# Optimization experiments

Measured on AMD Instinct MI355X. Metric: run time of the kernel, lower is better.

The kernel has to match this reference:

```python
import jax, jax.numpy as jnp
import numpy as np

B = 512
IMG = 32
NFF = 64
LAT_N = 256
LAT_C = 100
TOKEN_DIM = 3 + 2 * NFF  # 131
HEADS = 4
DEPTH = 2
MLP_HID = 4 * LAT_C
EPS = 1e-5


def _layernorm(x, g, b):
    mu = jnp.mean(x, axis=-1, keepdims=True)
    var = jnp.mean((x - mu) ** 2, axis=-1, keepdims=True)
    return (x - mu) * jax.lax.rsqrt(var + EPS) * g + b


def _mha(h, in_w, in_b, out_w, out_b):
    # torch nn.MultiheadAttention, batch_first, eval mode (no dropout)
    Bh, L, D = h.shape
    hd = D // HEADS
    qkv = h @ in_w.T + in_b  # [B, L, 3D]
    q, k, v = jnp.split(qkv, 3, axis=-1)
    def heads(t):
        return t.reshape(Bh, L, HEADS, hd).transpose(0, 2, 1, 3)  # [B,H,L,hd]
    q, k, v = heads(q), heads(k), heads(v)
    scores = jnp.einsum('bhqd,bhkd->bhqk', q, k) / jnp.sqrt(jnp.float32(hd))
    attn = jax.nn.softmax(scores, axis=-1)
    o = jnp.einsum('bhqk,bhkd->bhqd', attn, v)
    o = o.transpose(0, 2, 1, 3).reshape(Bh, L, D)
    return o @ out_w.T + out_b


def _forward(x, latents, latent_pos, fourier_matrix, proj_w, proj_b,
             q_w, q_b, k_w, k_b, v_w, v_b, o_w, o_b,
             ln1_g, ln1_b, attn_in_w, attn_in_b, attn_out_w, attn_out_b,
             ln2_g, ln2_b, mlp_w1, mlp_b1, mlp_w2, mlp_b2):
    Bx = x.shape[0]
    lat = (latents + latent_pos)[None].repeat(Bx, axis=0)  # [B, 256, 100]

    # per-pixel RGB tokens
    rgb = x.transpose(0, 2, 3, 1).reshape(Bx, -1, 3)  # [B, 1024, 3]

    # Fourier positional encoding
    yy, xx = jnp.meshgrid(jnp.arange(IMG, dtype=jnp.float32),
                          jnp.arange(IMG, dtype=jnp.float32), indexing='ij')
    coords = jnp.stack([xx / (IMG - 1), yy / (IMG - 1)], axis=-1).reshape(-1, 2)  # [1024, 2]
    proj = coords @ fourier_matrix  # [1024, NFF]
    pos = jnp.concatenate([jnp.cos(2 * jnp.pi * proj), jnp.sin(2 * jnp.pi * proj)], axis=-1)
    pos = jnp.broadcast_to(pos[None], (Bx, IMG * IMG, 2 * NFF))

    tokens = jnp.concatenate([rgb, pos], axis=-1)  # [B, 1024, 131]
    tokens = tokens @ proj_w.T + proj_b  # [B, 1024, 100]

    # K/V depend only on (fixed) tokens, identical across the 8 iterations
    k = tokens @ k_w.T + k_b
    v = tokens @ v_w.T + v_b

    scale = 1.0 / jnp.sqrt(jnp.float32(LAT_C))
    for _ in range(8):
        q = lat @ q_w.T + q_b  # [B, 256, 100]
        attn = jax.nn.softmax(jnp.einsum('bqc,bkc->bqk', q, k) * scale, axis=-1)
        lat = jnp.einsum('bqk,bkc->bqc', attn, v) @ o_w.T + o_b
        # latent transformer (depth=2, shared across the 8 iterations)
        for d in range(DEPTH):
            h = _layernorm(lat, ln1_g[d], ln1_b[d])
            lat = lat + _mha(h, attn_in_w[d], attn_in_b[d], attn_out_w[d], attn_out_b[d])
            h = _layernorm(lat, ln2_g[d], ln2_b[d])
            h = jax.nn.gelu(h @ mlp_w1[d].T + mlp_b1[d], approximate=False) @ mlp_w2[d].T + mlp_b2[d]
            lat = lat + h
    return lat.mean(axis=1)  # [B, 100]


def setup_inputs() -> dict:
    key = jax.random.key(0)
    ks = jax.random.split(key, 32)
    s = 0.02
    inp = {
        'x': jax.random.normal(ks[0], (B, 3, IMG, IMG), jnp.float32),
        'latents': jax.random.normal(ks[1], (LAT_N, LAT_C), jnp.float32),
        'latent_pos': jax.random.normal(ks[2], (LAT_N, LAT_C), jnp.float32),
        'fourier_matrix': jax.random.normal(ks[3], (2, NFF), jnp.float32),
        'proj_w': jax.random.normal(ks[4], (LAT_C, TOKEN_DIM), jnp.float32) * s,
        'proj_b': jnp.zeros((LAT_C,), jnp.float32),
        'q_w': jax.random.normal(ks[5], (LAT_C, LAT_C), jnp.float32) * s,
        'q_b': jnp.zeros((LAT_C,), jnp.float32),
        'k_w': jax.random.normal(ks[6], (LAT_C, LAT_C), jnp.float32) * s,
        'k_b': jnp.zeros((LAT_C,), jnp.float32),
        'v_w': jax.random.normal(ks[7], (LAT_C, LAT_C), jnp.float32) * s,
        'v_b': jnp.zeros((LAT_C,), jnp.float32),
        'o_w': jax.random.normal(ks[8], (LAT_C, LAT_C), jnp.float32) * s,
        'o_b': jnp.zeros((LAT_C,), jnp.float32),
        'ln1_g': jnp.ones((DEPTH, LAT_C), jnp.float32),
        'ln1_b': jnp.zeros((DEPTH, LAT_C), jnp.float32),
        'attn_in_w': jax.random.normal(ks[9], (DEPTH, 3 * LAT_C, LAT_C), jnp.float32) * s,
        'attn_in_b': jnp.zeros((DEPTH, 3 * LAT_C), jnp.float32),
        'attn_out_w': jax.random.normal(ks[10], (DEPTH, LAT_C, LAT_C), jnp.float32) * s,
        'attn_out_b': jnp.zeros((DEPTH, LAT_C), jnp.float32),
        'ln2_g': jnp.ones((DEPTH, LAT_C), jnp.float32),
        'ln2_b': jnp.zeros((DEPTH, LAT_C), jnp.float32),
        'mlp_w1': jax.random.normal(ks[11], (DEPTH, MLP_HID, LAT_C), jnp.float32) * s,
        'mlp_b1': jnp.zeros((DEPTH, MLP_HID), jnp.float32),
        'mlp_w2': jax.random.normal(ks[12], (DEPTH, LAT_C, MLP_HID), jnp.float32) * s,
        'mlp_b2': jnp.zeros((DEPTH, LAT_C), jnp.float32),
    }
    return inp


def reference(x, latents, latent_pos, fourier_matrix, proj_w, proj_b,
              q_w, q_b, k_w, k_b, v_w, v_b, o_w, o_b,
              ln1_g, ln1_b, attn_in_w, attn_in_b, attn_out_w, attn_out_b,
              ln2_g, ln2_b, mlp_w1, mlp_b1, mlp_w2, mlp_b2):
    return _forward(x, latents, latent_pos, fourier_matrix, proj_w, proj_b,
                    q_w, q_b, k_w, k_b, v_w, v_b, o_w, o_b,
                    ln1_g, ln1_b, attn_in_w, attn_in_b, attn_out_w, attn_out_b,
                    ln2_g, ln2_b, mlp_w1, mlp_b1, mlp_w2, mlp_b2)
```

## Files before the change

kernel.cpp:

```cpp
#include <hip/hip_runtime.h>
#include <cmath>

#define WS_AK 0
#define WS_AV 300
#define WS_U  600

#define UW_DK   0
#define UW_DV   106496
#define UW_QW   212992
#define UW_OW   227328
#define UW_W1   241664
#define UW_W2   344064
#define UW_AIW  444416
#define UW_AOW  542720
#define UW_WCNT 358400

typedef __attribute__((ext_vector_type(8))) short short8;
typedef __attribute__((ext_vector_type(4))) float f32x4;

#define MFMA(a, b, c) __builtin_amdgcn_mfma_f32_16x16x32_bf16((a), (b), (c), 0, 0, 0)

static __device__ __forceinline__ unsigned short f2bf(float f) {
  unsigned int u = __float_as_uint(f);
  u += 0x7FFF + ((u >> 16) & 1);
  return (unsigned short)(u >> 16);
}
static __device__ __forceinline__ float bf2f(unsigned short u) {
  return __uint_as_float(((unsigned int)u) << 16);
}
static __device__ __forceinline__ f32x4 zero4() { return (f32x4){0.f, 0.f, 0.f, 0.f}; }

__global__ void pre_amat_kernel(const float* __restrict__ proj_w,
                                const float* __restrict__ k_w,
                                const float* __restrict__ v_w,
                                float* __restrict__ ws) {
  int idx = blockIdx.x * blockDim.x + threadIdx.x;
  if (idx >= 600) return;
  int sel = idx / 300;
  int rem = idx % 300;
  int c = rem / 100, m = rem % 100;
  const float* w = sel ? v_w : k_w;
  float acc = 0.f;
  for (int n = 0; n < 100; ++n) acc += proj_w[n * 131 + c] * w[m * 100 + n];
  ws[(sel ? WS_AV : WS_AK) + c * 100 + m] = acc;
}

__global__ void pre_dmat_kernel(const float* __restrict__ fm,
                                const float* __restrict__ proj_w,
                                const float* __restrict__ proj_b,
                                const float* __restrict__ k_w,
                                const float* __restrict__ k_b,
                                const float* __restrict__ v_w,
                                const float* __restrict__ v_b,
                                unsigned short* __restrict__ uw) {
  __shared__ float pos[8][128];
  __shared__ float tc[8][100];
  int p0 = blockIdx.x * 8;
  int tid = threadIdx.x;
  for (int idx = tid; idx < 1024; idx += 256) {
    int pl = idx >> 7, f = idx & 127;
    int p = p0 + pl;
    float cx = (float)(p & 31) * (1.f / 31.f);
    float cy = (float)(p >> 5) * (1.f / 31.f);
    int fi = f & 63;
    float pr = cx * fm[fi] + cy * fm[64 + fi];
    float ang = 6.2831853071795864769f * pr;
    pos[pl][f] = (f < 64) ? cosf(ang) : sinf(ang);
  }
  __syncthreads();
  for (int idx = tid; idx < 800; idx += 256) {
    int pl = idx / 100, n = idx % 100;
    float acc = proj_b[n];
    const float* pw = proj_w + n * 131 + 3;
    for (int f = 0; f < 128; ++f) acc += pos[pl][f] * pw[f];
    tc[pl][n] = acc;
  }
  __syncthreads();
  for (int idx = tid; idx < 1600; idx += 256) {
    int sel = idx / 800;
    int rem = idx % 800;
    int pl = rem / 100, m = rem % 100;
    const float* w = sel ? v_w : k_w;
    float acc = sel ? v_b[m] : k_b[m];
    for (int n = 0; n < 100; ++n) acc += tc[pl][n] * w[m * 100 + n];
    if (sel) uw[UW_DV + m * 1024 + (p0 + pl)] = f2bf(acc);
    else     uw[UW_DK + (p0 + pl) * 104 + m] = f2bf(acc);
  }
  for (int idx = tid; idx < 32; idx += 256) {
    int pl = idx >> 2, mm = 100 + (idx & 3);
    uw[UW_DK + (p0 + pl) * 104 + mm] = 0;
  }
}

__global__ void pre_wfrag_kernel(const float* __restrict__ q_w,
                                 const float* __restrict__ o_w,
                                 const float* __restrict__ mlp_w1,
                                 const float* __restrict__ mlp_w2,
                                 const float* __restrict__ attn_in_w,
                                 const float* __restrict__ attn_out_w,
                                 unsigned short* __restrict__ uw) {
  int idx = blockIdx.x * 256 + threadIdx.x;
  if (idx >= UW_WCNT) return;
  float val = 0.f;
  if (idx < 14336) {
    int rem = idx;
    int kt = rem / 3584; rem %= 3584;
    int nt = rem / 512;  rem %= 512;
    int lane = rem >> 3, j = rem & 7;
    int k = kt * 32 + (lane >> 4) * 8 + j;
    int n = nt * 16 + (lane & 15);
    if (k < 100 && n < 100) val = q_w[n * 100 + k];
  } else if (idx < 28672) {
    int rem = idx - 14336;
    int kt = rem / 3584; rem %= 3584;
    int nt = rem / 512;  rem %= 512;
    int lane = rem >> 3, j = rem & 7;
    int k = kt * 32 + (lane >> 4) * 8 + j;
    int n = nt * 16 + (lane & 15);
    if (k < 100 && n < 100) val = o_w[n * 100 + k];
  } else if (idx < 131072) {
    int off = idx - 28672;
    int dd = off / 51200;
    int rem = off % 51200;
    int kt = rem / 12800; rem %= 12800;
    int nt = rem / 512;   rem %= 512;
    int lane = rem >> 3, j = rem & 7;
    int k = kt * 32 + (lane >> 4) * 8 + j;
    int n = nt * 16 + (lane & 15);
    if (k < 100) val = mlp_w1[dd * 40000 + n * 100 + k];
  } else if (idx < 231424) {
    int off = idx - 131072;
    int dd = off / 50176;
    int rem = off % 50176;
    int kt = rem / 3584; rem %= 3584;
    int nt = rem / 512;  rem %= 512;
    int lane = rem >> 3, j = rem & 7;
    int k = kt * 32 + (lane >> 4) * 8 + j;
    int n = nt * 16 + (lane & 15);
    if (k < 400 && n < 100) val = mlp_w2[dd * 40000 + n * 400 + k];
  } else if (idx < 329728) {
    int off = idx - 231424;
    int dw = off / 16384;
    int rem = off % 16384;
    int dd = dw / 3, wsel = dw % 3;
    int kt = rem / 4096; rem %= 4096;
    int nt = rem / 512;  rem %= 512;
    int lane = rem >> 3, j = rem & 7;
    int k = kt * 32 + (lane >> 4) * 8 + j;
    int np = nt * 16 + (lane & 15);
    int hh = np >> 5, dh = np & 31;
    if (k < 100 && dh < 25)
      val = attn_in_w[dd * 30000 + (wsel * 100 + hh * 25 + dh) * 100 + k];
  } else {
    int off = idx - 329728;
    int dd = off / 14336;
    int rem = off % 14336;
    int kt = rem / 3584; rem %= 3584;
    int nt = rem / 512;  rem %= 512;
    int lane = rem >> 3, j = rem & 7;
    int kp = kt * 32 + (lane >> 4) * 8 + j;
    int hh = kp >> 5, dh = kp & 31;
    int n = nt * 16 + (lane & 15);
    if (dh < 25 && n < 100)
      val = attn_out_w[dd * 10000 + n * 100 + hh * 25 + dh];
  }
  uw[UW_QW + idx] = f2bf(val);
}

__launch_bounds__(512, 4)
__global__ void perceiver_kernel(
    const float* __restrict__ x,
    const float* __restrict__ latents,
    const float* __restrict__ latent_pos,
    const float* __restrict__ q_b, const float* __restrict__ o_b,
    const float* __restrict__ ln1_g, const float* __restrict__ ln1_b,
    const float* __restrict__ attn_in_b, const float* __restrict__ attn_out_b,
    const float* __restrict__ ln2_g, const float* __restrict__ ln2_b,
    const float* __restrict__ mlp_b1, const float* __restrict__ mlp_b2,
    const float* __restrict__ ws,
    float* __restrict__ out) {
  __shared__ __align__(16) float s_pool[20208];
  float* s_sm = s_pool;
  float* Rf   = s_pool + 2800;
  unsigned short* R   = (unsigned short*)Rf;
  unsigned short* s_M = R;
  unsigned short* sK  = R;
  unsigned short* sV  = R + 8192;
  unsigned short* sP  = R + 15360;
  unsigned short* sQh   = R;
  unsigned short* kfrag = R + 9216;
  unsigned short* vfrag = R + 17408;
  unsigned short* sPm   = R + 25600;

  const int tid  = threadIdx.x;
  const int b    = blockIdx.x;
  const int lane = tid & 63;
  const int wv   = tid >> 6;
  const int li   = lane & 15;
  const int lg   = lane >> 4;
  const unsigned short* uw = (const unsigned short*)(ws + WS_U);

  for (int i = tid; i < 200; i += 512) {
    s_sm[i] = ln1_g[i]; s_sm[200 + i] = ln1_b[i];
    s_sm[400 + i] = ln2_g[i]; s_sm[600 + i] = ln2_b[i];
  }
  for (int i = tid; i < 600; i += 512) s_sm[800 + i] = attn_in_b[i];
  for (int i = tid; i < 800; i += 512) s_sm[1400 + i] = mlp_b1[i];
  for (int i = tid; i < 300; i += 512) { s_sm[2200 + i] = ws[WS_AK + i]; s_sm[2500 + i] = ws[WS_AV + i]; }

  f32x4 latC[2][7];
  #pragma unroll
  for (int mt2 = 0; mt2 < 2; ++mt2)
    #pragma unroll
    for (int nt = 0; nt < 7; ++nt) {
      const int col = nt * 16 + li;
      #pragma unroll
      for (int rg = 0; rg < 4; ++rg) {
        const int row = (2 * wv + mt2) * 16 + lg * 4 + rg;
        latC[mt2][nt][rg] = (col < 100)
            ? latents[row * 100 + col] + latent_pos[row * 100 + col] : 0.f;
      }
    }

  const float* xb = x + (long)b * 3072;

  auto ln_stage = [&](const float* gg, const float* bb) {
    #pragma unroll
    for (int mt2 = 0; mt2 < 2; ++mt2)
      #pragma unroll
      for (int rg = 0; rg < 4; ++rg) {
        float s = 0.f, sq = 0.f;
        #pragma unroll
        for (int nt = 0; nt < 7; ++nt) {
          const int col = nt * 16 + li;
          if (col < 100) { const float v = latC[mt2][nt][rg]; s += v; sq += v * v; }
        }
        s += __shfl_xor(s, 1); sq += __shfl_xor(sq, 1);
        s += __shfl_xor(s, 2); sq += __shfl_xor(sq, 2);
        s += __shfl_xor(s, 4); sq += __shfl_xor(sq, 4);
        s += __shfl_xor(s, 8); sq += __shfl_xor(sq, 8);
        const float mu = s * 0.01f;
        const float rs = rsqrtf(sq * 0.01f - mu * mu + 1e-5f);
        const int row = (2 * wv + mt2) * 16 + lg * 4 + rg;
        #pragma unroll
        for (int nt = 0; nt < 7; ++nt) {
          const int col = nt * 16 + li;
          s_M[row * 132 + col] = (col < 100)
              ? f2bf((latC[mt2][nt][rg] - mu) * rs * gg[col] + bb[col]) : 0;
        }
        s_M[row * 132 + 112 + li] = 0;
      }
  };

  for (int it = 0; it < 8; ++it) {
    #pragma unroll
    for (int mt2 = 0; mt2 < 2; ++mt2)
      #pragma unroll
      for (int rg = 0; rg < 4; ++rg) {
        const int row = (2 * wv + mt2) * 16 + lg * 4 + rg;
        #pragma unroll
        for (int nt = 0; nt < 7; ++nt) {
          const int col = nt * 16 + li;
          s_M[row * 132 + col] = (col < 100) ? f2bf(latC[mt2][nt][rg]) : 0;
        }
        s_M[row * 132 + 112 + li] = 0;
      }

    {
      short8 aq[2][4];
      #pragma unroll
      for (int mt2 = 0; mt2 < 2; ++mt2)
        #pragma unroll
        for (int kt = 0; kt < 4; ++kt)
          aq[mt2][kt] = *(const short8*)(s_M + ((2 * wv + mt2) * 16 + li) * 132 + kt * 32 + lg * 8);
      #pragma unroll
      for (int nt = 0; nt < 7; ++nt) {
        f32x4 a0 = zero4(), a1 = zero4();
        #pragma unroll
        for (int kt = 0; kt < 4; ++kt) {
          short8 bw = *(const short8*)(uw + UW_QW + ((kt * 7 + nt) * 64 + lane) * 8);
          a0 = MFMA(aq[0][kt], bw, a0);
          a1 = MFMA(aq[1][kt], bw, a1);
        }
        const int col = nt * 16 + li;
        const float qb = (col < 100) ? q_b[col] : 0.f;
        #pragma unroll
        for (int rg = 0; rg < 4; ++rg) {
          const int r0 = (2 * wv) * 16 + lg * 4 + rg;
          const int r1 = (2 * wv + 1) * 16 + lg * 4 + rg;
          s_M[r0 * 132 + col] = (col < 100) ? f2bf((a0[rg] + qb) * 0.1f) : 0;
          s_M[r1 * 132 + col] = (col < 100) ? f2bf((a1[rg] + qb) * 0.1f) : 0;
        }
      }
    }

    short8 aq2[2][4];
    #pragma unroll
    for (int mt2 = 0; mt2 < 2; ++mt2)
      #pragma unroll
      for (int kt = 0; kt < 4; ++kt)
        aq2[mt2][kt] = *(const short8*)(s_M + ((2 * wv + mt2) * 16 + li) * 132 + kt * 32 + lg * 8);

    f32x4 O[2][7];
    #pragma unroll
    for (int a0 = 0; a0 < 2; ++a0)
      #pragma unroll
      for (int a1 = 0; a1 < 7; ++a1) O[a0][a1] = zero4();

    for (int t0 = 0; t0 < 1024; t0 += 64) {
      __syncthreads();
      for (int vi = tid; vi < 1024; vi += 512) {
        const int key = vi & 63, cg = vi >> 6;
        const int p = t0 + key;
        short8 w;
        if (cg < 13) {
          const float xr = xb[p], xg = xb[1024 + p], xv = xb[2048 + p];
          short8 dk = *(const short8*)(uw + UW_DK + p * 104 + cg * 8);
          #pragma unroll
          for (int e = 0; e < 8; ++e) {
            const int c = cg * 8 + e;
            float val = 0.f;
            if (c < 100)
              val = xr * s_sm[2200 + c] + xg * s_sm[2300 + c] + xv * s_sm[2400 + c]
                  + bf2f((unsigned short)dk[e]);
            w[e] = (short)f2bf(val);
          }
        } else {
          #pragma unroll
          for (int e = 0; e < 8; ++e) w[e] = 0;
        }
        *(short8*)(sK + vi * 8) = w;
      }
      for (int vi = tid; vi < 896; vi += 512) {
        const int ch = vi % 112, kg = vi / 112;
        const int pv0 = t0 + kg * 8;
        short8 w;
        if (ch < 100) {
          const float4 xr0 = *(const float4*)(xb + pv0);
          const float4 xr1 = *(const float4*)(xb + pv0 + 4);
          const float4 xg0 = *(const float4*)(xb + 1024 + pv0);
          const float4 xg1 = *(const float4*)(xb + 1024 + pv0 + 4);
          const float4 xv0 = *(const float4*)(xb + 2048 + pv0);
          const float4 xv1 = *(const float4*)(xb + 2048 + pv0 + 4);
          short8 dv = *(const short8*)(uw + UW_DV + ch * 1024 + pv0);
          const float a0 = s_sm[2500 + ch], a1 = s_sm[2600 + ch], a2 = s_sm[2700 + ch];
          const float xrv[8] = {xr0.x, xr0.y, xr0.z, xr0.w, xr1.x, xr1.y, xr1.z, xr1.w};
          const float xgv[8] = {xg0.x, xg0.y, xg0.z, xg0.w, xg1.x, xg1.y, xg1.z, xg1.w};
          const float xvv[8] = {xv0.x, xv0.y, xv0.z, xv0.w, xv1.x, xv1.y, xv1.z, xv1.w};
          #pragma unroll
          for (int e = 0; e < 8; ++e)
            w[e] = (short)f2bf(xrv[e] * a0 + xgv[e] * a1 + xvv[e] * a2
                               + bf2f((unsigned short)dv[e]));
        } else if (ch == 100) {
          #pragma unroll
          for (int e = 0; e < 8; ++e) w[e] = (short)0x3F80;
        } else {
          #pragma unroll
          for (int e = 0; e < 8; ++e) w[e] = 0;
        }
        *(short8*)(sV + vi * 8) = w;
      }
      __syncthreads();

      #pragma unroll
      for (int ntk = 0; ntk < 4; ++ntk) {
        f32x4 s0 = zero4(), s1 = zero4();
        #pragma unroll
        for (int kt = 0; kt < 4; ++kt) {
          short8 bk = *(const short8*)(sK + ((kt * 4 + lg) * 64 + ntk * 16 + li) * 8);
          s0 = MFMA(aq2[0][kt], bk, s0);
          s1 = MFMA(aq2[1][kt], bk, s1);
        }
        #pragma unroll
        for (int rg = 0; rg < 4; ++rg) {
          const int r0 = (2 * wv) * 16 + lg * 4 + rg;
          const int r1 = (2 * wv + 1) * 16 + lg * 4 + rg;
          sP[r0 * 76 + ntk * 16 + li] = f2bf(__expf(s0[rg]));
          sP[r1 * 76 + ntk * 16 + li] = f2bf(__expf(s1[rg]));
        }
      }
      short8 ap[2][2];
      #pragma unroll
      for (int mt2 = 0; mt2 < 2; ++mt2)
        #pragma unroll
        for (int kt2 = 0; kt2 < 2; ++kt2)
          ap[mt2][kt2] = *(const short8*)(sP + ((2 * wv + mt2) * 16 + li) * 76 + kt2 * 32 + lg * 8);
      #pragma unroll
      for (int nt = 0; nt < 7; ++nt) {
        short8 bv0 = *(const short8*)(sV + ((0 + lg) * 112 + nt * 16 + li) * 8);
        short8 bv1 = *(const short8*)(sV + ((4 + lg) * 112 + nt * 16 + li) * 8);
        #pragma unroll
        for (int mt2 = 0; mt2 < 2; ++mt2) {
          O[mt2][nt] = MFMA(ap[mt2][0], bv0, O[mt2][nt]);
          O[mt2][nt] = MFMA(ap[mt2][1], bv1, O[mt2][nt]);
        }
      }
    }
    __syncthreads();

    #pragma unroll
    for (int mt2 = 0; mt2 < 2; ++mt2)
      #pragma unroll
      for (int rg = 0; rg < 4; ++rg) {
        const float lv = __shfl(O[mt2][6][rg], (lane & 48) + 4);
        const float linv = 1.0f / lv;
        const int row = (2 * wv + mt2) * 16 + lg * 4 + rg;
        #pragma unroll
        for (int nt = 0; nt < 7; ++nt) {
          const int col = nt * 16 + li;
          s_M[row * 132 + col] = (col < 100) ? f2bf(O[mt2][nt][rg] * linv) : 0;
        }
        s_M[row * 132 + 112 + li] = 0;
      }

    {
      short8 ao[2][4];
      #pragma unroll
      for (int mt2 = 0; mt2 < 2; ++mt2)
        #pragma unroll
        for (int kt = 0; kt < 4; ++kt)
          ao[mt2][kt] = *(const short8*)(s_M + ((2 * wv + mt2) * 16 + li) * 132 + kt * 32 + lg * 8);
      #pragma unroll
      for (int nt = 0; nt < 7; ++nt) {
        f32x4 a0 = zero4(), a1 = zero4();
        #pragma unroll
        for (int kt = 0; kt < 4; ++kt) {
          short8 bw = *(const short8*)(uw + UW_OW + ((kt * 7 + nt) * 64 + lane) * 8);
          a0 = MFMA(ao[0][kt], bw, a0);
          a1 = MFMA(ao[1][kt], bw, a1);
        }
        const int col = nt * 16 + li;
        const float ob = (col < 100) ? o_b[col] : 0.f;
        #pragma unroll
        for (int rg = 0; rg < 4; ++rg) {
          latC[0][nt][rg] = (col < 100) ? a0[rg] + ob : 0.f;
          latC[1][nt][rg] = (col < 100) ? a1[rg] + ob : 0.f;
        }
      }
    }

    for (int d = 0; d < 2; ++d) {
      ln_stage(&s_sm[d * 100], &s_sm[200 + d * 100]);
      short8 ah[2][4];
      #pragma unroll
      for (int mt2 = 0; mt2 < 2; ++mt2)
        #pragma unroll
        for (int kt = 0; kt < 4; ++kt)
          ah[mt2][kt] = *(const short8*)(s_M + ((2 * wv + mt2) * 16 + li) * 132 + kt * 32 + lg * 8);

      f32x4 co[2][7];
      #pragma unroll
      for (int nt = 0; nt < 7; ++nt) {
        const int col = nt * 16 + li;
        const float ob = (col < 100) ? attn_out_b[d * 100 + col] : 0.f;
        #pragma unroll
        for (int rg = 0; rg < 4; ++rg) {
          co[0][nt][rg] = (col < 100) ? latC[0][nt][rg] + ob : 0.f;
          co[1][nt][rg] = (col < 100) ? latC[1][nt][rg] + ob : 0.f;
        }
      }

      for (int h = 0; h < 4; ++h) {
        __syncthreads();
        #pragma unroll
        for (int ntd = 0; ntd < 2; ++ntd) {
          f32x4 cq0 = zero4(), cq1 = zero4(), ck0 = zero4(), ck1 = zero4(),
                cv0 = zero4(), cv1 = zero4();
          #pragma unroll
          for (int kt = 0; kt < 4; ++kt) {
            const int bidx = ((kt * 8 + h * 2 + ntd) * 64 + lane) * 8;
            short8 bq  = *(const short8*)(uw + UW_AIW + (d * 3 + 0) * 16384 + bidx);
            short8 bkk = *(const short8*)(uw + UW_AIW + (d * 3 + 1) * 16384 + bidx);
            short8 bvv = *(const short8*)(uw + UW_AIW + (d * 3 + 2) * 16384 + bidx);
            cq0 = MFMA(ah[0][kt], bq,  cq0); cq1 = MFMA(ah[1][kt], bq,  cq1);
            ck0 = MFMA(ah[0][kt], bkk, ck0); ck1 = MFMA(ah[1][kt], bkk, ck1);
            cv0 = MFMA(ah[0][kt], bvv, cv0); cv1 = MFMA(ah[1][kt], bvv, cv1);
          }
          const int dh = ntd * 16 + li;
          const bool ok = dh < 25;
          const float qb2 = ok ? s_sm[800 + d * 300 +       h * 25 + dh] : 0.f;
          const float kb2 = ok ? s_sm[800 + d * 300 + 100 + h * 25 + dh] : 0.f;
          const float vb2 = ok ? s_sm[800 + d * 300 + 200 + h * 25 + dh] : 0.f;
          #pragma unroll
          for (int mt2 = 0; mt2 < 2; ++mt2)
            #pragma unroll
            for (int rg = 0; rg < 4; ++rg) {
              const int rr = lg * 4 + rg;
              const int row = (2 * wv + mt2) * 16 + rr;
              const float q = mt2 ? cq1[rg] : cq0[rg];
              const float k = mt2 ? ck1[rg] : ck0[rg];
              const float v = mt2 ? cv1[rg] : cv0[rg];
              sQh[row * 36 + dh] = ok ? f2bf((q + qb2) * 0.2f) : 0;
              kfrag[((2 * wv + mt2) * 64 + (dh >> 3) * 16 + rr) * 8 + (dh & 7)] =
                  ok ? f2bf(k + kb2) : 0;
              vfrag[((wv * 2 + ntd) * 64 + (mt2 * 2 + (rr >> 3)) * 16 + li) * 8 + (rr & 7)] =
                  ok ? f2bf(v + vb2) : (unsigned short)((dh == 25) ? 0x3F80 : 0);
            }
        }
        __syncthreads();

        short8 aqh0 = *(const short8*)(sQh + ((2 * wv + 0) * 16 + li) * 36 + lg * 8);
        short8 aqh1 = *(const short8*)(sQh + ((2 * wv + 1) * 16 + li) * 36 + lg * 8);
        f32x4 Oh00 = zero4(), Oh01 = zero4(), Oh10 = zero4(), Oh11 = zero4();
        for (int t = 0; t < 8; ++t) {
          short8 bk0 = *(const short8*)(kfrag + ((t * 2 + 0) * 64 + lane) * 8);
          short8 bk1 = *(const short8*)(kfrag + ((t * 2 + 1) * 64 + lane) * 8);
          f32x4 s00 = MFMA(aqh0, bk0, zero4());
          f32x4 s01 = MFMA(aqh0, bk1, zero4());
          f32x4 s10 = MFMA(aqh1, bk0, zero4());
          f32x4 s11 = MFMA(aqh1, bk1, zero4());
          #pragma unroll
          for (int rg = 0; rg < 4; ++rg) {
            const int r0 = (2 * wv) * 16 + lg * 4 + rg;
            const int r1 = (2 * wv + 1) * 16 + lg * 4 + rg;
            sPm[r0 * 36 + li]      = f2bf(__expf(s00[rg]));
            sPm[r0 * 36 + 16 + li] = f2bf(__expf(s01[rg]));
            sPm[r1 * 36 + li]      = f2bf(__expf(s10[rg]));
            sPm[r1 * 36 + 16 + li] = f2bf(__expf(s11[rg]));
          }
          short8 ap0 = *(const short8*)(sPm + ((2 * wv + 0) * 16 + li) * 36 + lg * 8);
          short8 ap1 = *(const short8*)(sPm + ((2 * wv + 1) * 16 + li) * 36 + lg * 8);
          short8 bv0 = *(const short8*)(vfrag + ((t * 2 + 0) * 64 + lane) * 8);
          short8 bv1 = *(const short8*)(vfrag + ((t * 2 + 1) * 64 + lane) * 8);
          Oh00 = MFMA(ap0, bv0, Oh00); Oh01 = MFMA(ap0, bv1, Oh01);
          Oh10 = MFMA(ap1, bv0, Oh10); Oh11 = MFMA(ap1, bv1, Oh11);
        }
        #pragma unroll
        for (int mt2 = 0; mt2 < 2; ++mt2)
          #pragma unroll
          for (int rg = 0; rg < 4; ++rg) {
            const f32x4& o0 = mt2 ? Oh10 : Oh00;
            const f32x4& o1 = mt2 ? Oh11 : Oh01;
            const float lv = __shfl(o1[rg], (lane & 48) + 9);
            const float linv = 1.0f / lv;
            const int row = (2 * wv + mt2) * 16 + lg * 4 + rg;
            sPm[row * 36 + li]      = (li < 25)      ? f2bf(o0[rg] * linv) : 0;
            sPm[row * 36 + 16 + li] = (16 + li < 25) ? f2bf(o1[rg] * linv) : 0;
          }
        short8 ao0 = *(const short8*)(sPm + ((2 * wv + 0) * 16 + li) * 36 + lg * 8);
        short8 ao1 = *(const short8*)(sPm + ((2 * wv + 1) * 16 + li) * 36 + lg * 8);
        #pragma unroll
        for (int nt = 0; nt < 7; ++nt) {
          short8 bw = *(const short8*)(uw + UW_AOW + d * 14336 + ((h * 7 + nt) * 64 + lane) * 8);
          co[0][nt] = MFMA(ao0, bw, co[0][nt]);
          co[1][nt] = MFMA(ao1, bw, co[1][nt]);
        }
      }
      __syncthreads();

      #pragma unroll
      for (int mt2 = 0; mt2 < 2; ++mt2)
        #pragma unroll
        for (int nt = 0; nt < 7; ++nt) latC[mt2][nt] = co[mt2][nt];

      ln_stage(&s_sm[400 + d * 100], &s_sm[600 + d * 100]);
      short8 ahm[2][4];
      #pragma unroll
      for (int mt2 = 0; mt2 < 2; ++mt2)
        #pragma unroll
        for (int kt = 0; kt < 4; ++kt)
          ahm[mt2][kt] = *(const short8*)(s_M + ((2 * wv + mt2) * 16 + li) * 132 + kt * 32 + lg * 8);

      f32x4 c2[2][7];
      #pragma unroll
      for (int nt = 0; nt < 7; ++nt) {
        const int col = nt * 16 + li;
        const float b2 = (col < 100) ? mlp_b2[d * 100 + col] : 0.f;
        #pragma unroll
        for (int rg = 0; rg < 4; ++rg) {
          c2[0][nt][rg] = (col < 100) ? latC[0][nt][rg] + b2 : 0.f;
          c2[1][nt][rg] = (col < 100) ? latC[1][nt][rg] + b2 : 0.f;
        }
      }

      const int w1off = UW_W1 + d * 51200;
      const int w2off = UW_W2 + d * 50176;
      for (int chunk = 0; chunk < 3; ++chunk) {
        #pragma unroll
        for (int ntl = 0; ntl < 8; ++ntl) {
          f32x4 a0 = zero4(), a1 = zero4();
          #pragma unroll
          for (int kt = 0; kt < 4; ++kt) {
            short8 bw = *(const short8*)(uw + w1off + ((kt * 25 + (chunk * 8 + ntl)) * 64 + lane) * 8);
            a0 = MFMA(ahm[0][kt], bw, a0);
            a1 = MFMA(ahm[1][kt], bw, a1);
          }
          const int col = ntl * 16 + li;
          const float bias = s_sm[1400 + d * 400 + chunk * 128 + col];
          #pragma unroll
          for (int rg = 0; rg < 4; ++rg) {
            const int r0 = (2 * wv) * 16 + lg * 4 + rg;
            const int r1 = (2 * wv + 1) * 16 + lg * 4 + rg;
            float h0 = a0[rg] + bias, h1 = a1[rg] + bias;
            s_M[r0 * 132 + col] = f2bf(0.5f * h0 * (1.0f + erff(h0 * 0.70710678118654752f)));
            s_M[r1 * 132 + col] = f2bf(0.5f * h1 * (1.0f + erff(h1 * 0.70710678118654752f)));
          }
        }
        #pragma unroll
        for (int ktl = 0; ktl < 4; ++ktl) {
          short8 ahh0 = *(const short8*)(s_M + ((2 * wv + 0) * 16 + li) * 132 + ktl * 32 + lg * 8);
          short8 ahh1 = *(const short8*)(s_M + ((2 * wv + 1) * 16 + li) * 132 + ktl * 32 + lg * 8);
          #pragma unroll
          for (int nt = 0; nt < 7; ++nt) {
            short8 bw = *(const short8*)(uw + w2off + (((chunk * 4 + ktl) * 7 + nt) * 64 + lane) * 8);
            c2[0][nt] = MFMA(ahh0, bw, c2[0][nt]);
            c2[1][nt] = MFMA(ahh1, bw, c2[1][nt]);
          }
        }
      }
      {
        f32x4 a0 = zero4(), a1 = zero4();
        #pragma unroll
        for (int kt = 0; kt < 4; ++kt) {
          short8 bw = *(const short8*)(uw + w1off + ((kt * 25 + 24) * 64 + lane) * 8);
          a0 = MFMA(ahm[0][kt], bw, a0);
          a1 = MFMA(ahm[1][kt], bw, a1);
        }
        const float bias = s_sm[1400 + d * 400 + 384 + li];
        #pragma unroll
        for (int rg = 0; rg < 4; ++rg) {
          const int r0 = (2 * wv) * 16 + lg * 4 + rg;
          const int r1 = (2 * wv + 1) * 16 + lg * 4 + rg;
          float h0 = a0[rg] + bias, h1 = a1[rg] + bias;
          s_M[r0 * 132 + li] = f2bf(0.5f * h0 * (1.0f + erff(h0 * 0.70710678118654752f)));
          s_M[r1 * 132 + li] = f2bf(0.5f * h1 * (1.0f + erff(h1 * 0.70710678118654752f)));
          s_M[r0 * 132 + 16 + li] = 0;
          s_M[r1 * 132 + 16 + li] = 0;
        }
        short8 ahh0 = *(const short8*)(s_M + ((2 * wv + 0) * 16 + li) * 132 + lg * 8);
        short8 ahh1 = *(const short8*)(s_M + ((2 * wv + 1) * 16 + li) * 132 + lg * 8);
        #pragma unroll
        for (int nt = 0; nt < 7; ++nt) {
          short8 bw = *(const short8*)(uw + w2off + ((12 * 7 + nt) * 64 + lane) * 8);
          c2[0][nt] = MFMA(ahh0, bw, c2[0][nt]);
          c2[1][nt] = MFMA(ahh1, bw, c2[1][nt]);
        }
      }
      #pragma unroll
      for (int mt2 = 0; mt2 < 2; ++mt2)
        #pragma unroll
        for (int nt = 0; nt < 7; ++nt) latC[mt2][nt] = c2[mt2][nt];
    }
  }

  __syncthreads();
  #pragma unroll
  for (int nt = 0; nt < 7; ++nt) {
    float v = 0.f;
    #pragma unroll
    for (int rg = 0; rg < 4; ++rg) v += latC[0][nt][rg] + latC[1][nt][rg];
    v += __shfl_xor(v, 16);
    v += __shfl_xor(v, 32);
    if (lg == 0) Rf[wv * 112 + nt * 16 + li] = v;
  }
  __syncthreads();
  if (tid < 100) {
    float s = 0.f;
    #pragma unroll
    for (int w = 0; w < 8; ++w) s += Rf[w * 112 + tid];
    out[b * 100 + tid] = s * (1.0f / 256.0f);
  }
}

extern "C" void kernel_launch(void* const* d_in, const int* in_sizes, int n_in,
                              void* d_out, int out_size, void* d_ws, size_t ws_size,
                              hipStream_t stream) {
  (void)in_sizes; (void)n_in; (void)out_size; (void)ws_size;
  const float* x          = (const float*)d_in[0];
  const float* latents    = (const float*)d_in[1];
  const float* latent_pos = (const float*)d_in[2];
  const float* fm         = (const float*)d_in[3];
  const float* proj_w     = (const float*)d_in[4];
  const float* proj_b     = (const float*)d_in[5];
  const float* q_w        = (const float*)d_in[6];
  const float* q_b        = (const float*)d_in[7];
  const float* k_w        = (const float*)d_in[8];
  const float* k_b        = (const float*)d_in[9];
  const float* v_w        = (const float*)d_in[10];
  const float* v_b        = (const float*)d_in[11];
  const float* o_w        = (const float*)d_in[12];
  const float* o_b        = (const float*)d_in[13];
  const float* ln1_g      = (const float*)d_in[14];
  const float* ln1_b      = (const float*)d_in[15];
  const float* attn_in_w  = (const float*)d_in[16];
  const float* attn_in_b  = (const float*)d_in[17];
  const float* attn_out_w = (const float*)d_in[18];
  const float* attn_out_b = (const float*)d_in[19];
  const float* ln2_g      = (const float*)d_in[20];
  const float* ln2_b      = (const float*)d_in[21];
  const float* mlp_w1     = (const float*)d_in[22];
  const float* mlp_b1     = (const float*)d_in[23];
  const float* mlp_w2     = (const float*)d_in[24];
  const float* mlp_b2     = (const float*)d_in[25];
  float* ws   = (float*)d_ws;
  float* outp = (float*)d_out;
  unsigned short* uw = (unsigned short*)(ws + WS_U);

  pre_amat_kernel<<<3, 256, 0, stream>>>(proj_w, k_w, v_w, ws);
  pre_dmat_kernel<<<128, 256, 0, stream>>>(fm, proj_w, proj_b, k_w, k_b, v_w, v_b, uw);
  pre_wfrag_kernel<<<(UW_WCNT + 255) / 256, 256, 0, stream>>>(
      q_w, o_w, mlp_w1, mlp_w2, attn_in_w, attn_out_w, uw);
  perceiver_kernel<<<512, 512, 0, stream>>>(
      x, latents, latent_pos, q_b, o_b,
      ln1_g, ln1_b, attn_in_b, attn_out_b,
      ln2_g, ln2_b, mlp_b1, mlp_b2, ws, outp);
}
```

Baseline: 5.538 ms.

## Fold rgb K/V contributions algebraically and stream MFMA-ready K/V fragments from global

K and V were previously rebuilt per batch element in shared memory every tile as rgb·A plus a position-dependent bf16 term. The new path splits the score and output algebraically. The rgb part of Q·K becomes a small precomputed Q·A_K term added per key. The rgb part of P·V is accumulated as the P-weighted rgb sums and applied after the loop. The position-only K/V are prelaid in MFMA fragment order in global memory and loaded directly, which removes the per-tile shared-memory staging and both block barriers. Each wave now uses a private P buffer, in exchange for more global/L2 traffic on fragment loads and extra register state.

Result: slower. 10.04 ms (+81.3%).

```diff
diff --git a/kernel.cpp b/kernel.cpp
--- a/kernel.cpp
+++ b/kernel.cpp
@@ -5,14 +5,15 @@
 #define WS_AV 300
 #define WS_U  600
 
-#define UW_DK   0
-#define UW_DV   106496
-#define UW_QW   212992
-#define UW_OW   227328
-#define UW_W1   241664
-#define UW_W2   344064
-#define UW_AIW  444416
-#define UW_AOW  542720
+#define UW_DKT 0
+#define UW_DVT 131072
+#define UW_AKT 245760
+#define UW_QW  247808
+#define UW_OW  262144
+#define UW_W1  276480
+#define UW_W2  378880
+#define UW_AIW 479232
+#define UW_AOW 577536
 #define UW_WCNT 358400
 
 typedef __attribute__((ext_vector_type(8))) short short8;
@@ -24,9 +25,6 @@
   unsigned int u = __float_as_uint(f);
   u += 0x7FFF + ((u >> 16) & 1);
   return (unsigned short)(u >> 16);
-}
-static __device__ __forceinline__ float bf2f(unsigned short u) {
-  return __uint_as_float(((unsigned int)u) << 16);
 }
 static __device__ __forceinline__ f32x4 zero4() { return (f32x4){0.f, 0.f, 0.f, 0.f}; }
 
@@ -43,6 +41,35 @@
   float acc = 0.f;
   for (int n = 0; n < 100; ++n) acc += proj_w[n * 131 + c] * w[m * 100 + n];
   ws[(sel ? WS_AV : WS_AK) + c * 100 + m] = acc;
+}
+
+__global__ void pre_akt_kernel(const float* __restrict__ ws,
+                               unsigned short* __restrict__ uw) {
+  int idx = blockIdx.x * blockDim.x + threadIdx.x;
+  if (idx >= 2048) return;
+  int kt = idx >> 9, lane = (idx >> 3) & 63, j = idx & 7;
+  int k = kt * 32 + (lane >> 4) * 8 + j;
+  int n = lane & 15;
+  float val = (k < 100 && n < 3) ? ws[WS_AK + n * 100 + k] : 0.f;
+  uw[UW_AKT + idx] = f2bf(val);
+}
+
+__global__ void pre_fill_kernel(unsigned short* __restrict__ uw) {
+  int idx = blockIdx.x * blockDim.x + threadIdx.x;
+  if (idx >= 40960) return;
+  if (idx < 28672) {
+    int m = 100 + idx % 28, p = idx / 28;
+    int kt = m >> 5, ng = p >> 4;
+    int lane = (((m & 31) >> 3) << 4) + (p & 15);
+    uw[UW_DKT + ((kt * 64 + ng) * 64 + lane) * 8 + (m & 7)] = 0;
+  } else {
+    int r = idx - 28672;
+    int m = 100 + r % 12, p = r / 12;
+    int kv = p >> 5, nt = m >> 4;
+    int lane = (((p & 31) >> 3) << 4) + (m & 15);
+    uw[UW_DVT + ((kv * 7 + nt) * 64 + lane) * 8 + (p & 7)] =
+        (m == 100) ? (unsigned short)0x3F80 : (unsigned short)0;
+  }
 }
 
 __global__ void pre_dmat_kernel(const float* __restrict__ fm,
@@ -80,15 +107,19 @@
     int sel = idx / 800;
     int rem = idx % 800;
     int pl = rem / 100, m = rem % 100;
+    int p = p0 + pl;
     const float* w = sel ? v_w : k_w;
     float acc = sel ? v_b[m] : k_b[m];
     for (int n = 0; n < 100; ++n) acc += tc[pl][n] * w[m * 100 + n];
-    if (sel) uw[UW_DV + m * 1024 + (p0 + pl)] = f2bf(acc);
-    else     uw[UW_DK + (p0 + pl) * 104 + m] = f2bf(acc);
-  }
-  for (int idx = tid; idx < 32; idx += 256) {
-    int pl = idx >> 2, mm = 100 + (idx & 3);
-    uw[UW_DK + (p0 + pl) * 104 + mm] = 0;
+    if (sel) {
+      int kv = p >> 5, nt = m >> 4;
+      int lane = (((p & 31) >> 3) << 4) + (m & 15);
+      uw[UW_DVT + ((kv * 7 + nt) * 64 + lane) * 8 + (p & 7)] = f2bf(acc);
+    } else {
+      int kt = m >> 5, ng = p >> 4;
+      int lane = (((m & 31) >> 3) << 4) + (p & 15);
+      uw[UW_DKT + ((kt * 64 + ng) * 64 + lane) * 8 + (m & 7)] = f2bf(acc);
+    }
   }
 }
 
@@ -179,14 +210,11 @@
     const float* __restrict__ mlp_b1, const float* __restrict__ mlp_b2,
     const float* __restrict__ ws,
     float* __restrict__ out) {
-  __shared__ __align__(16) float s_pool[20208];
+  __shared__ __align__(16) float s_pool[19908];
   float* s_sm = s_pool;
-  float* Rf   = s_pool + 2800;
+  float* Rf   = s_pool + 2500;
   unsigned short* R   = (unsigned short*)Rf;
   unsigned short* s_M = R;
-  unsigned short* sK  = R;
-  unsigned short* sV  = R + 8192;
-  unsigned short* sP  = R + 15360;
   unsigned short* sQh   = R;
   unsigned short* kfrag = R + 9216;
   unsigned short* vfrag = R + 17408;
@@ -199,6 +227,7 @@
   const int li   = lane & 15;
   const int lg   = lane >> 4;
   const unsigned short* uw = (const unsigned short*)(ws + WS_U);
+  unsigned short* sPw = R + wv * 4224;
 
   for (int i = tid; i < 200; i += 512) {
     s_sm[i] = ln1_g[i]; s_sm[200 + i] = ln1_b[i];
@@ -206,7 +235,8 @@
   }
   for (int i = tid; i < 600; i += 512) s_sm[800 + i] = attn_in_b[i];
   for (int i = tid; i < 800; i += 512) s_sm[1400 + i] = mlp_b1[i];
-  for (int i = tid; i < 300; i += 512) { s_sm[2200 + i] = ws[WS_AK + i]; s_sm[2500 + i] = ws[WS_AV + i]; }
+  for (int i = tid; i < 300; i += 512) s_sm[2200 + i] = ws[WS_AV + i];
+  __syncthreads();
 
   f32x4 latC[2][7];
   #pragma unroll
@@ -301,102 +331,100 @@
       for (int kt = 0; kt < 4; ++kt)
         aq2[mt2][kt] = *(const short8*)(s_M + ((2 * wv + mt2) * 16 + li) * 132 + kt * 32 + lg * 8);
 
+    f32x4 qa0v = zero4(), qa1v = zero4();
+    #pragma unroll
+    for (int kt = 0; kt < 4; ++kt) {
+      short8 bw = *(const short8*)(uw + UW_AKT + (kt * 64 + lane) * 8);
+      qa0v = MFMA(aq2[0][kt], bw, qa0v);
+      qa1v = MFMA(aq2[1][kt], bw, qa1v);
+    }
+
     f32x4 O[2][7];
     #pragma unroll
     for (int a0 = 0; a0 < 2; ++a0)
       #pragma unroll
       for (int a1 = 0; a1 < 7; ++a1) O[a0][a1] = zero4();
+    float pxa[2][4][3];
+    #pragma unroll
+    for (int a0 = 0; a0 < 2; ++a0)
+      #pragma unroll
+      for (int a1 = 0; a1 < 4; ++a1)
+        #pragma unroll
+        for (int a2 = 0; a2 < 3; ++a2) pxa[a0][a1][a2] = 0.f;
 
     for (int t0 = 0; t0 < 1024; t0 += 64) {
-      __syncthreads();
-      for (int vi = tid; vi < 1024; vi += 512) {
-        const int key = vi & 63, cg = vi >> 6;
-        const int p = t0 + key;
-        short8 w;
-        if (cg < 13) {
-          const float xr = xb[p], xg = xb[1024 + p], xv = xb[2048 + p];
-          short8 dk = *(const short8*)(uw + UW_DK + p * 104 + cg * 8);
-          #pragma unroll
-          for (int e = 0; e < 8; ++e) {
-            const int c = cg * 8 + e;
-            float val = 0.f;
-            if (c < 100)
-              val = xr * s_sm[2200 + c] + xg * s_sm[2300 + c] + xv * s_sm[2400 + c]
-                  + bf2f((unsigned short)dk[e]);
-            w[e] = (short)f2bf(val);
-          }
-        } else {
-          #pragma unroll
-          for (int e = 0; e < 8; ++e) w[e] = 0;
-        }
-        *(short8*)(sK + vi * 8) = w;
-      }
-      for (int vi = tid; vi < 896; vi += 512) {
-        const int ch = vi % 112, kg = vi / 112;
-        const int pv0 = t0 + kg * 8;
-        short8 w;
-        if (ch < 100) {
-          const float4 xr0 = *(const float4*)(xb + pv0);
-          const float4 xr1 = *(const float4*)(xb + pv0 + 4);
-          const float4 xg0 = *(const float4*)(xb + 1024 + pv0);
-          const float4 xg1 = *(const float4*)(xb + 1024 + pv0 + 4);
-          const float4 xv0 = *(const float4*)(xb + 2048 + pv0);
-          const float4 xv1 = *(const float4*)(xb + 2048 + pv0 + 4);
-          short8 dv = *(const short8*)(uw + UW_DV + ch * 1024 + pv0);
-          const float a0 = s_sm[2500 + ch], a1 = s_sm[2600 + ch], a2 = s_sm[2700 + ch];
-          const float xrv[8] = {xr0.x, xr0.y, xr0.z, xr0.w, xr1.x, xr1.y, xr1.z, xr1.w};
-          const float xgv[8] = {xg0.x, xg0.y, xg0.z, xg0.w, xg1.x, xg1.y, xg1.z, xg1.w};
-          const float xvv[8] = {xv0.x, xv0.y, xv0.z, xv0.w, xv1.x, xv1.y, xv1.z, xv1.w};
-          #pragma unroll
-          for (int e = 0; e < 8; ++e)
-            w[e] = (short)f2bf(xrv[e] * a0 + xgv[e] * a1 + xvv[e] * a2
-                               + bf2f((unsigned short)dv[e]));
-        } else if (ch == 100) {
-          #pragma unroll
-          for (int e = 0; e < 8; ++e) w[e] = (short)0x3F80;
-        } else {
-          #pragma unroll
-          for (int e = 0; e < 8; ++e) w[e] = 0;
-        }
-        *(short8*)(sV + vi * 8) = w;
-      }
-      __syncthreads();
-
+      float qa3[2][4][3];
+      #pragma unroll
+      for (int rg = 0; rg < 4; ++rg)
+        #pragma unroll
+        for (int ch = 0; ch < 3; ++ch) {
+          qa3[0][rg][ch] = __shfl(qa0v[rg], (lane & 48) + ch);
+          qa3[1][rg][ch] = __shfl(qa1v[rg], (lane & 48) + ch);
+        }
       #pragma unroll
       for (int ntk = 0; ntk < 4; ++ntk) {
         f32x4 s0 = zero4(), s1 = zero4();
         #pragma unroll
         for (int kt = 0; kt < 4; ++kt) {
-          short8 bk = *(const short8*)(sK + ((kt * 4 + lg) * 64 + ntk * 16 + li) * 8);
+          short8 bk = *(const short8*)(uw + UW_DKT + ((kt * 64 + (t0 >> 4) + ntk) * 64 + lane) * 8);
           s0 = MFMA(aq2[0][kt], bk, s0);
           s1 = MFMA(aq2[1][kt], bk, s1);
         }
+        const int p = t0 + ntk * 16 + li;
+        const float xr = xb[p], xg = xb[1024 + p], xv = xb[2048 + p];
         #pragma unroll
         for (int rg = 0; rg < 4; ++rg) {
-          const int r0 = (2 * wv) * 16 + lg * 4 + rg;
-          const int r1 = (2 * wv + 1) * 16 + lg * 4 + rg;
-          sP[r0 * 76 + ntk * 16 + li] = f2bf(__expf(s0[rg]));
-          sP[r1 * 76 + ntk * 16 + li] = f2bf(__expf(s1[rg]));
-        }
-      }
-      short8 ap[2][2];
-      #pragma unroll
-      for (int mt2 = 0; mt2 < 2; ++mt2)
-        #pragma unroll
-        for (int kt2 = 0; kt2 < 2; ++kt2)
-          ap[mt2][kt2] = *(const short8*)(sP + ((2 * wv + mt2) * 16 + li) * 76 + kt2 * 32 + lg * 8);
+          float sv0 = s0[rg] + qa3[0][rg][0] * xr + qa3[0][rg][1] * xg + qa3[0][rg][2] * xv;
+          float sv1 = s1[rg] + qa3[1][rg][0] * xr + qa3[1][rg][1] * xg + qa3[1][rg][2] * xv;
+          float pe0 = __expf(sv0);
+          float pe1 = __expf(sv1);
+          pxa[0][rg][0] += pe0 * xr; pxa[0][rg][1] += pe0 * xg; pxa[0][rg][2] += pe0 * xv;
+          pxa[1][rg][0] += pe1 * xr; pxa[1][rg][1] += pe1 * xg; pxa[1][rg][2] += pe1 * xv;
+          sPw[(lg * 4 + rg) * 76 + ntk * 16 + li]        = f2bf(pe0);
+          sPw[(16 + lg * 4 + rg) * 76 + ntk * 16 + li]   = f2bf(pe1);
+        }
+      }
+      short8 ap00 = *(const short8*)(sPw + li * 76 + lg * 8);
+      short8 ap01 = *(const short8*)(sPw + li * 76 + 32 + lg * 8);
+      short8 ap10 = *(const short8*)(sPw + (16 + li) * 76 + lg * 8);
+      short8 ap11 = *(const short8*)(sPw + (16 + li) * 76 + 32 + lg * 8);
+      const int kv = t0 >> 5;
       #pragma unroll
       for (int nt = 0; nt < 7; ++nt) {
-        short8 bv0 = *(const short8*)(sV + ((0 + lg) * 112 + nt * 16 + li) * 8);
-        short8 bv1 = *(const short8*)(sV + ((4 + lg) * 112 + nt * 16 + li) * 8);
-        #pragma unroll
-        for (int mt2 = 0; mt2 < 2; ++mt2) {
-          O[mt2][nt] = MFMA(ap[mt2][0], bv0, O[mt2][nt]);
-          O[mt2][nt] = MFMA(ap[mt2][1], bv1, O[mt2][nt]);
-        }
+        short8 bv0 = *(const short8*)(uw + UW_DVT + ((kv * 7 + nt) * 64 + lane) * 8);
+        short8 bv1 = *(const short8*)(uw + UW_DVT + (((kv + 1) * 7 + nt) * 64 + lane) * 8);
+        O[0][nt] = MFMA(ap00, bv0, O[0][nt]);
+        O[0][nt] = MFMA(ap01, bv1, O[0][nt]);
+        O[1][nt] = MFMA(ap10, bv0, O[1][nt]);
+        O[1][nt] = MFMA(ap11, bv1, O[1][nt]);
       }
     }
-    __syncthreads();
+
+    #pragma unroll
+    for (int mt2 = 0; mt2 < 2; ++mt2)
+      #pragma unroll
+      for (int rg = 0; rg < 4; ++rg)
+        #pragma unroll
+        for (int ch = 0; ch < 3; ++ch) {
+          float v = pxa[mt2][rg][ch];
+          v += __shfl_xor(v, 1);
+          v += __shfl_xor(v, 2);
+          v += __shfl_xor(v, 4);
+          v += __shfl_xor(v, 8);
+          pxa[mt2][rg][ch] = v;
+        }
+    #pragma unroll
+    for (int mt2 = 0; mt2 < 2; ++mt2)
+      #pragma unroll
+      for (int nt = 0; nt < 7; ++nt) {
+        const int col = nt * 16 + li;
+        if (col < 100) {
+          const float av0 = s_sm[2200 + col], av1 = s_sm[2300 + col], av2 = s_sm[2400 + col];
+          #pragma unroll
+          for (int rg = 0; rg < 4; ++rg)
+            O[mt2][nt][rg] += pxa[mt2][rg][0] * av0 + pxa[mt2][rg][1] * av1 + pxa[mt2][rg][2] * av2;
+        }
+      }
 
     #pragma unroll
     for (int mt2 = 0; mt2 < 2; ++mt2)
@@ -697,7 +725,9 @@
   unsigned short* uw = (unsigned short*)(ws + WS_U);
 
   pre_amat_kernel<<<3, 256, 0, stream>>>(proj_w, k_w, v_w, ws);
+  pre_akt_kernel<<<8, 256, 0, stream>>>(ws, uw);
   pre_dmat_kernel<<<128, 256, 0, stream>>>(fm, proj_w, proj_b, k_w, k_b, v_w, v_b, uw);
+  pre_fill_kernel<<<160, 256, 0, stream>>>(uw);
   pre_wfrag_kernel<<<(UW_WCNT + 255) / 256, 256, 0, stream>>>(
       q_w, o_w, mlp_w1, mlp_w2, attn_in_w, attn_out_w, uw);
   perceiver_kernel<<<512, 512, 0, stream>>>(
```
